# Kernel optimization log

Measured on AMD Instinct MI355X. Metric: run time of the kernel, lower is better.

The kernel has to match this reference:

```python
import jax, jax.numpy as jnp
import numpy as np

RATIO = 0.3
BN_EPS = 1e-5
L2_EPS = 1e-8


def setup_inputs() -> dict:
    key = jax.random.key(0)
    ks = jax.random.split(key, 16)
    B, N, D, E = 128, 577, 512, 1024
    H = E // 2  # mlp hidden = 512
    s = lambda k, shp, fan: jax.random.normal(k, shp, dtype=jnp.float32) * (1.0 / np.sqrt(fan))
    return {
        "features": jax.random.normal(ks[0], (B, N, D), dtype=jnp.float32),
        "atten": jax.random.uniform(ks[1], (B, N), dtype=jnp.float32),
        # image_weight_generator: Linear(D,D) -> ReLU -> Linear(D,1)
        "wg_w1": s(ks[2], (D, D), D), "wg_b1": jnp.zeros((D,), jnp.float32),
        "wg_w2": s(ks[3], (D, 1), D), "wg_b2": jnp.zeros((1,), jnp.float32),
        # fc: Linear(D, E)
        "fc_w": s(ks[4], (D, E), D), "fc_b": jnp.zeros((E,), jnp.float32),
        # MLP: Linear(D,H) -> BN(H) -> ReLU -> Linear(H,E)
        "mlp_w0": s(ks[5], (D, H), D), "mlp_b0": jnp.zeros((H,), jnp.float32),
        "bn_g": jnp.ones((H,), jnp.float32), "bn_b": jnp.zeros((H,), jnp.float32),
        "mlp_w1": s(ks[6], (H, E), H), "mlp_b1": jnp.zeros((E,), jnp.float32),
    }


def reference(features, atten, wg_w1, wg_b1, wg_w2, wg_b2, fc_w, fc_b,
              mlp_w0, mlp_b0, bn_g, bn_b, mlp_w1, mlp_b1):
    k = int((atten.shape[1] - 1) * RATIO)  # static: int(576*0.3)=172
    # weight-generator MLP -> per-token scalar weights [B, N]
    h = jax.nn.relu(jnp.einsum('bnd,de->bne', features, wg_w1) + wg_b1)
    w = (jnp.einsum('bnd,do->bno', h, wg_w2) + wg_b2)[..., 0]
    w = w.at[:, 0].set(-jnp.inf)  # mask CLS token
    w = jax.nn.softmax(w, axis=1)
    # top-k token selection (sorted indices), batched gather
    _, idx = jax.lax.top_k(w, k)                      # [B, k]
    idx = jnp.sort(idx, axis=1)
    sel = jnp.take_along_axis(features, idx[:, :, None], axis=1)  # [B, k, D]
    # l2norm over feature dim
    norm = jnp.sqrt(jnp.sum(sel * sel, axis=-1, keepdims=True)) + L2_EPS
    sel = sel / norm
    # fc in half precision (original: fc(selected_tokens.half()))
    feats = (sel.astype(jnp.float16) @ fc_w.astype(jnp.float16)
             + fc_b.astype(jnp.float16))              # [B, k, E] fp16
    # MLP with training-mode BatchNorm over flattened (B*k) dim
    B, K, D = sel.shape
    x = sel.reshape(B * K, D) @ mlp_w0 + mlp_b0       # [B*k, H]
    mean = jnp.mean(x, axis=0)
    var = jnp.mean((x - mean) ** 2, axis=0)
    x = (x - mean) * jax.lax.rsqrt(var + BN_EPS) * bn_g + bn_b
    x = jax.nn.relu(x)
    x = (x @ mlp_w1 + mlp_b1).reshape(B, K, -1)       # [B, k, E]
    return (x + feats.astype(jnp.float32)).astype(jnp.float32)
```

## Files before the change

### kernel.cpp

```cpp
#include <hip/hip_runtime.h>
#include <hip/hip_fp16.h>
#include <math.h>

#define B_    128
#define NTOK  577
#define KSEL  172
#define M_WG  (B_*NTOK)
#define M_SEL (B_*KSEL)
#define DELTA 8e-3f

typedef float f32x4 __attribute__((ext_vector_type(4)));
typedef short s16x8 __attribute__((ext_vector_type(8)));
typedef short s16x4 __attribute__((ext_vector_type(4)));
typedef _Float16 f16x8 __attribute__((ext_vector_type(8)));

__device__ __forceinline__ void gll16(const void* g, void* l) {
    __builtin_amdgcn_global_load_lds(
        (const __attribute__((address_space(1))) unsigned int*)g,
        (__attribute__((address_space(3))) unsigned int*)l, 16, 0, 0);
}

__global__ void zero_kernel(float* __restrict__ w, float* __restrict__ stats) {
    int i = blockIdx.x * 256 + threadIdx.x;
    if (i < M_WG) w[i] = 0.f;
    if (i < 1024) stats[i] = 0.f;
}

__global__ __launch_bounds__(256) void transpose_f16_kernel(
    const float* __restrict__ wgw1, const float* __restrict__ mw0,
    const float* __restrict__ mw1, const float* __restrict__ fcw,
    short* __restrict__ w1t, short* __restrict__ w0t,
    short* __restrict__ mw1t, short* __restrict__ fct)
{
    const int z = blockIdx.z;
    const float* src; short* dst; int N;
    if (z == 0)      { src = wgw1; dst = w1t;  N = 512;  }
    else if (z == 1) { src = mw0;  dst = w0t;  N = 512;  }
    else if (z == 2) { src = mw1;  dst = mw1t; N = 1024; }
    else             { src = fcw;  dst = fct;  N = 1024; }
    const int n0 = blockIdx.x * 64;
    if (n0 >= N) return;
    const int k0 = blockIdx.y * 64;
    __shared__ float t[64][65];
    const int tid = threadIdx.x;
#pragma unroll
    for (int rr = 0; rr < 16; rr++) {
        int kl = rr * 4 + (tid >> 6), nl = tid & 63;
        t[kl][nl] = src[(size_t)(k0 + kl) * N + n0 + nl];
    }
    __syncthreads();
    const int nl = tid >> 2, kc = tid & 3;
    short hs[16];
#pragma unroll
    for (int j = 0; j < 16; j++)
        hs[j] = (short)__half_as_ushort(__float2half(t[kc * 16 + j][nl]));
    size_t o = (size_t)(n0 + nl) * 512 + k0 + kc * 16;
    *(s16x8*)(dst + o)     = *(s16x8*)hs;
    *(s16x8*)(dst + o + 8) = *(s16x8*)(hs + 8);
}

__global__ __launch_bounds__(256) void wg_f16_kernel(
    const float* __restrict__ F, const short* __restrict__ W1t,
    const float* __restrict__ b1, const float* __restrict__ v,
    float* __restrict__ w_out)
{
    __shared__ short A2[2][4096];
    __shared__ short B2[2][8192];
    const int tid = threadIdx.x, lane = tid & 63, wn = tid >> 6;
    const int r = lane & 15, kq = lane >> 4;
    const int rowbase = blockIdx.y * 128, nbase = blockIdx.x * 256;
    float av[2][8];

    {
        int k0 = 0;
#pragma unroll
        for (int p = 0; p < 4; p++) {
            int c = tid + p * 256, col = c & 255, kqs = c >> 8;
            gll16(W1t + (size_t)(nbase + col) * 512 + k0 + kqs * 8, &B2[0][c * 8]);
        }
#pragma unroll
        for (int p = 0; p < 2; p++) {
            int c = tid + p * 256, row = c & 127, kqs = c >> 7;
            const float* s = F + (size_t)(rowbase + row) * 512 + k0 + kqs * 8;
            f32x4 u0 = *(const f32x4*)s, u1 = *(const f32x4*)(s + 4);
#pragma unroll
            for (int j = 0; j < 4; j++) { av[p][j] = u0[j]; av[p][4 + j] = u1[j]; }
            short hs[8];
#pragma unroll
            for (int j = 0; j < 8; j++) hs[j] = (short)__half_as_ushort(__float2half(av[p][j]));
            *(s16x8*)&A2[0][kqs * 1024 + row * 8] = *(s16x8*)hs;
        }
    }
    __syncthreads();

    f32x4 acc[8][4];
#pragma unroll
    for (int i = 0; i < 8; i++)
#pragma unroll
        for (int j = 0; j < 4; j++) acc[i][j] = (f32x4)(0.0f);

    for (int km = 0; km < 16; km++) {
        const int pb = km & 1;
        if (km < 15) {
            int k0 = (km + 1) * 32;
#pragma unroll
            for (int p = 0; p < 4; p++) {
                int c = tid + p * 256, col = c & 255, kqs = c >> 8;
                gll16(W1t + (size_t)(nbase + col) * 512 + k0 + kqs * 8, &B2[pb ^ 1][c * 8]);
            }
#pragma unroll
            for (int p = 0; p < 2; p++) {
                int c = tid + p * 256, row = c & 127, kqs = c >> 7;
                const float* s = F + (size_t)(rowbase + row) * 512 + k0 + kqs * 8;
                f32x4 u0 = *(const f32x4*)s, u1 = *(const f32x4*)(s + 4);
#pragma unroll
                for (int j = 0; j < 4; j++) { av[p][j] = u0[j]; av[p][4 + j] = u1[j]; }
            }
        }
        f16x8 bfrag[4];
#pragma unroll
        for (int nf = 0; nf < 4; nf++)
            bfrag[nf] = *(const f16x8*)&B2[pb][kq * 2048 + (wn * 64 + nf * 16 + r) * 8];
#pragma unroll
        for (int mf = 0; mf < 8; mf++) {
            f16x8 a = *(const f16x8*)&A2[pb][kq * 1024 + (mf * 16 + r) * 8];
#pragma unroll
            for (int nf = 0; nf < 4; nf++)
                acc[mf][nf] = __builtin_amdgcn_mfma_f32_16x16x32_f16(a, bfrag[nf], acc[mf][nf], 0, 0, 0);
        }
        if (km < 15) {
#pragma unroll
            for (int p = 0; p < 2; p++) {
                int c = tid + p * 256, row = c & 127, kqs = c >> 7;
                short hs[8];
#pragma unroll
                for (int j = 0; j < 8; j++) hs[j] = (short)__half_as_ushort(__float2half(av[p][j]));
                *(s16x8*)&A2[pb ^ 1][kqs * 1024 + row * 8] = *(s16x8*)hs;
            }
        }
        __syncthreads();
    }

    float b1v[4], vv[4];
#pragma unroll
    for (int nf = 0; nf < 4; nf++) {
        int col = nbase + wn * 64 + nf * 16 + r;
        b1v[nf] = b1[col]; vv[nf] = v[col];
    }
#pragma unroll
    for (int mf = 0; mf < 8; mf++)
#pragma unroll
        for (int i = 0; i < 4; i++) {
            float s = 0.f;
#pragma unroll
            for (int nf = 0; nf < 4; nf++)
                s += fmaxf(acc[mf][nf][i] + b1v[nf], 0.f) * vv[nf];
            s += __shfl_xor(s, 1); s += __shfl_xor(s, 2);
            s += __shfl_xor(s, 4); s += __shfl_xor(s, 8);
            if (r == 0)
                atomicAdd(&w_out[rowbase + mf * 16 + kq * 4 + i], s);
        }
}

__global__ __launch_bounds__(512) void topk2_kernel(
    const float* __restrict__ w, int* __restrict__ cin, int* __restrict__ unc,
    int* __restrict__ meta)
{
    __shared__ float sval[1024];
    __shared__ int   sidx[1024];
    __shared__ int mcnt, ucnt;
    __shared__ float thr_s;
    const int b = blockIdx.x;
    const int tid = threadIdx.x;
    for (int i = tid; i < 1024; i += 512) {
        if (i < 576) { sval[i] = w[b * NTOK + 1 + i]; sidx[i] = 1 + i; }
        else         { sval[i] = -1e38f;              sidx[i] = 0x7fffffff; }
    }
    __syncthreads();
    for (int ksz = 2; ksz <= 1024; ksz <<= 1) {
        for (int j = ksz >> 1; j > 0; j >>= 1) {
            int i = ((tid & ~(j - 1)) << 1) | (tid & (j - 1));
            int ixj = i | j;
            float va = sval[i], vb = sval[ixj];
            int ia = sidx[i], ib = sidx[ixj];
            bool a_first = (va > vb) || (va == vb && ia < ib);
            bool dirDesc = ((i & ksz) == 0);
            bool doswap = dirDesc ? (!a_first) : a_first;
            if (doswap) { sval[i] = vb; sval[ixj] = va; sidx[i] = ib; sidx[ixj] = ia; }
            __syncthreads();
        }
    }
    if (tid == 0) { thr_s = sval[KSEL - 1]; mcnt = 0; ucnt = 0; }
    __syncthreads();
    const float thr = thr_s;
    for (int i = tid; i < 576; i += 512) {
        float vv = sval[i]; int id = sidx[i];
        if (vv > thr + DELTA) {
            int p = atomicAdd(&mcnt, 1);
            cin[b * KSEL + p] = id;
        } else if (vv >= thr - DELTA) {
            int p = atomicAdd(&ucnt, 1);
            if (p < 256) unc[b * 256 + p] = id;
        }
    }
    __syncthreads();
    if (tid == 0) {
        int m = mcnt;
        int u = (ucnt < 256) ? ucnt : 256;
        meta[b * 4]     = m;
        meta[b * 4 + 1] = KSEL - m;
        meta[b * 4 + 2] = u;
    }
}

__global__ __launch_bounds__(256) void refine_kernel(
    const float* __restrict__ F, const float* __restrict__ W1,
    const float* __restrict__ b1, const float* __restrict__ v,
    const int* __restrict__ unc, const int* __restrict__ meta,
    float* __restrict__ rscore)
{
    const int b = blockIdx.y, tid = threadIdx.x;
    const int u = meta[b * 4 + 2];
    __shared__ float fr[512];
    __shared__ float redbuf[4];
    for (int s = blockIdx.x; s < u; s += 32) {
        int tok = unc[b * 256 + s];
        __syncthreads();
        fr[tid]       = F[((size_t)b * NTOK + tok) * 512 + tid];
        fr[tid + 256] = F[((size_t)b * NTOK + tok) * 512 + tid + 256];
        __syncthreads();
        float a0 = b1[tid], a1 = b1[tid + 256];
#pragma unroll 4
        for (int k = 0; k < 512; k++) {
            float fk = fr[k];
            a0 = fmaf(fk, W1[(size_t)k * 512 + tid], a0);
            a1 = fmaf(fk, W1[(size_t)k * 512 + tid + 256], a1);
        }
        float p = fmaxf(a0, 0.f) * v[tid] + fmaxf(a1, 0.f) * v[tid + 256];
#pragma unroll
        for (int off = 32; off > 0; off >>= 1) p += __shfl_down(p, off);
        if ((tid & 63) == 0) redbuf[tid >> 6] = p;
        __syncthreads();
        if (tid == 0) rscore[b * 256 + s] = redbuf[0] + redbuf[1] + redbuf[2] + redbuf[3];
    }
}

__global__ __launch_bounds__(256) void select_kernel(
    const int* __restrict__ cin, const int* __restrict__ unc,
    const float* __restrict__ rscore, const int* __restrict__ meta,
    int* __restrict__ idx_out)
{
    const int b = blockIdx.x, tid = threadIdx.x;
    const int m = meta[b * 4], u = meta[b * 4 + 2];
    __shared__ float uval[256];
    __shared__ int   uidx[256];
    __shared__ int   fin[256];
    if (tid < u) { uval[tid] = rscore[b * 256 + tid]; uidx[tid] = unc[b * 256 + tid]; }
    else         { uval[tid] = -1e38f;                uidx[tid] = 0x7fffffff; }
    __syncthreads();
    for (int ksz = 2; ksz <= 256; ksz <<= 1) {
        for (int j = ksz >> 1; j > 0; j >>= 1) {
            if (tid < 128) {
                int i = ((tid & ~(j - 1)) << 1) | (tid & (j - 1));
                int ixj = i | j;
                float va = uval[i], vb = uval[ixj];
                int ia = uidx[i], ib = uidx[ixj];
                bool a_first = (va > vb) || (va == vb && ia < ib);
                bool dirDesc = ((i & ksz) == 0);
                if (dirDesc ? !a_first : a_first) {
                    uval[i] = vb; uval[ixj] = va; uidx[i] = ib; uidx[ixj] = ia;
                }
            }
            __syncthreads();
        }
    }
    if (tid < m) fin[tid] = cin[b * KSEL + tid];
    else if (tid < KSEL) fin[tid] = uidx[tid - m];
    else fin[tid] = 0x7fffffff;
    __syncthreads();
    for (int ksz = 2; ksz <= 256; ksz <<= 1) {
        for (int j = ksz >> 1; j > 0; j >>= 1) {
            if (tid < 128) {
                int i = ((tid & ~(j - 1)) << 1) | (tid & (j - 1));
                int ixj = i | j;
                int a = fin[i], bb = fin[ixj];
                bool asc = ((i & ksz) == 0);
                if (asc ? (a > bb) : (a < bb)) { fin[i] = bb; fin[ixj] = a; }
            }
            __syncthreads();
        }
    }
    if (tid < KSEL) idx_out[b * KSEL + tid] = fin[tid];
}

__global__ __launch_bounds__(128) void gather_norm_kernel(
    const float* __restrict__ F, const int* __restrict__ idx,
    short* __restrict__ Sh)
{
    const int g = blockIdx.x;
    const int b = g / KSEL;
    const int tok = idx[g];
    const float4* src = (const float4*)(F + ((size_t)b * NTOK + tok) * 512);
    const int t = threadIdx.x;
    float4 v = src[t];
    float ss = v.x * v.x + v.y * v.y + v.z * v.z + v.w * v.w;
#pragma unroll
    for (int off = 32; off > 0; off >>= 1) ss += __shfl_down(ss, off);
    __shared__ float red[2];
    if ((t & 63) == 0) red[t >> 6] = ss;
    __syncthreads();
    float inv = 1.0f / (sqrtf(red[0] + red[1]) + 1e-8f);
    float xs[4] = {v.x * inv, v.y * inv, v.z * inv, v.w * inv};
    short hs[4];
#pragma unroll
    for (int j = 0; j < 4; j++) hs[j] = (short)__half_as_ushort(__float2half(xs[j]));
    *(s16x4*)(Sh + (size_t)g * 512 + t * 4) = *(s16x4*)hs;
}

__global__ __launch_bounds__(256) void gemm_x1_kernel(
    const short* __restrict__ Sh, const short* __restrict__ W0t,
    const float* __restrict__ b0, short* __restrict__ X1h, float* __restrict__ stats)
{
    __shared__ short A[4096], Bt[8192];
    const int tid = threadIdx.x, lane = tid & 63, wn = tid >> 6;
    const int rowbase = blockIdx.y * 128, nbase = blockIdx.x * 256;
    const int r = lane & 15, kq = lane >> 4;
    f32x4 acc[8][4];
#pragma unroll
    for (int i = 0; i < 8; i++)
#pragma unroll
        for (int j = 0; j < 4; j++) acc[i][j] = (f32x4)(0.0f);
    for (int k0 = 0; k0 < 512; k0 += 32) {
#pragma unroll
        for (int p = 0; p < 2; p++) {
            int c = tid + p * 256, row = c & 127, kqs = c >> 7;
            gll16(Sh + (size_t)(rowbase + row) * 512 + k0 + kqs * 8, A + c * 8);
        }
#pragma unroll
        for (int p = 0; p < 4; p++) {
            int c = tid + p * 256, col = c & 255, kqs = c >> 8;
            gll16(W0t + (size_t)(nbase + col) * 512 + k0 + kqs * 8, Bt + c * 8);
        }
        __syncthreads();
        f16x8 b[4];
#pragma unroll
        for (int nf = 0; nf < 4; nf++)
            b[nf] = *(const f16x8*)(Bt + kq * 2048 + (wn * 64 + nf * 16 + r) * 8);
#pragma unroll
        for (int mf = 0; mf < 8; mf++) {
            f16x8 a = *(const f16x8*)(A + kq * 1024 + (mf * 16 + r) * 8);
#pragma unroll
            for (int nf = 0; nf < 4; nf++)
                acc[mf][nf] = __builtin_amdgcn_mfma_f32_16x16x32_f16(a, b[nf], acc[mf][nf], 0, 0, 0);
        }
        __syncthreads();
    }
#pragma unroll
    for (int nf = 0; nf < 4; nf++) {
        int col = nbase + wn * 64 + nf * 16 + r;
        float b0v = b0[col];
        float cs = 0.f, cq = 0.f;
#pragma unroll
        for (int mf = 0; mf < 8; mf++)
#pragma unroll
            for (int i = 0; i < 4; i++) {
                int row = rowbase + mf * 16 + kq * 4 + i;
                float val = acc[mf][nf][i] + b0v;
                X1h[(size_t)row * 512 + col] = (short)__half_as_ushort(__float2half(val));
                cs += val; cq += val * val;
            }
        cs += __shfl_xor(cs, 16); cs += __shfl_xor(cs, 32);
        cq += __shfl_xor(cq, 16); cq += __shfl_xor(cq, 32);
        if (kq == 0) {
            atomicAdd(&stats[col], cs);
            atomicAdd(&stats[512 + col], cq);
        }
    }
}

__global__ void bn_finalize_kernel(const float* __restrict__ stats,
                                   const float* __restrict__ g,
                                   const float* __restrict__ b,
                                   float* __restrict__ ss)
{
    int c = threadIdx.x;
    float mean = stats[c] * (1.0f / M_SEL);
    float var = stats[512 + c] * (1.0f / M_SEL) - mean * mean;
    float sc = g[c] * rsqrtf(var + 1e-5f);
    ss[c] = sc;
    ss[512 + c] = b[c] - mean * sc;
}

__global__ __launch_bounds__(256) void gemm_out2_kernel(
    const short* __restrict__ Sh, const short* __restrict__ FCt,
    const float* __restrict__ fcb, const short* __restrict__ X1h,
    const short* __restrict__ W1t, const float* __restrict__ ssbuf,
    const float* __restrict__ b1, float* __restrict__ out)
{
    __shared__ short A2[2][4096];
    __shared__ short B2[2][8192];
    __shared__ float sc[512], sh_[512];
    const int tid = threadIdx.x, lane = tid & 63, wn = tid >> 6;
    const int rowbase = blockIdx.y * 128, nbase = blockIdx.x * 256;
    const int r = lane & 15, kq = lane >> 4;
    for (int i = tid; i < 512; i += 256) { sc[i] = ssbuf[i]; sh_[i] = ssbuf[512 + i]; }
    f32x4 acc[8][4];
#pragma unroll
    for (int i = 0; i < 8; i++)
#pragma unroll
        for (int j = 0; j < 4; j++) acc[i][j] = (f32x4)(0.0f);

    {
#pragma unroll
        for (int p = 0; p < 2; p++) {
            int c = tid + p * 256, row = c & 127, kqs = c >> 7;
            gll16(Sh + (size_t)(rowbase + row) * 512 + kqs * 8, &A2[0][c * 8]);
        }
#pragma unroll
        for (int p = 0; p < 4; p++) {
            int c = tid + p * 256, col = c & 255, kqs = c >> 8;
            gll16(FCt + (size_t)(nbase + col) * 512 + kqs * 8, &B2[0][c * 8]);
        }
    }
    __syncthreads();
    for (int km = 0; km < 16; km++) {
        const int pb = km & 1;
        if (km < 15) {
            int k0 = (km + 1) * 32;
#pragma unroll
            for (int p = 0; p < 2; p++) {
                int c = tid + p * 256, row = c & 127, kqs = c >> 7;
                gll16(Sh + (size_t)(rowbase + row) * 512 + k0 + kqs * 8, &A2[pb ^ 1][c * 8]);
            }
#pragma unroll
            for (int p = 0; p < 4; p++) {
                int c = tid + p * 256, col = c & 255, kqs = c >> 8;
                gll16(FCt + (size_t)(nbase + col) * 512 + k0 + kqs * 8, &B2[pb ^ 1][c * 8]);
            }
        }
        f16x8 b[4];
#pragma unroll
        for (int nf = 0; nf < 4; nf++)
            b[nf] = *(const f16x8*)&B2[pb][kq * 2048 + (wn * 64 + nf * 16 + r) * 8];
#pragma unroll
        for (int mf = 0; mf < 8; mf++) {
            f16x8 a = *(const f16x8*)&A2[pb][kq * 1024 + (mf * 16 + r) * 8];
#pragma unroll
            for (int nf = 0; nf < 4; nf++)
                acc[mf][nf] = __builtin_amdgcn_mfma_f32_16x16x32_f16(a, b[nf], acc[mf][nf], 0, 0, 0);
        }
        __syncthreads();
    }
#pragma unroll
    for (int nf = 0; nf < 4; nf++) {
        float fb = __half2float(__float2half(fcb[nbase + wn * 64 + nf * 16 + r]));
#pragma unroll
        for (int mf = 0; mf < 8; mf++)
#pragma unroll
            for (int i = 0; i < 4; i++) {
                float t = __half2float(__float2half(acc[mf][nf][i]));
                acc[mf][nf][i] = __half2float(__float2half(t + fb));
            }
    }

    s16x8 xv[2];
    {
#pragma unroll
        for (int p = 0; p < 2; p++) {
            int c = tid + p * 256, row = c & 127, kqs = c >> 7;
            xv[p] = *(const s16x8*)(X1h + (size_t)(rowbase + row) * 512 + kqs * 8);
        }
#pragma unroll
        for (int p = 0; p < 2; p++) {
            int c = tid + p * 256, row = c & 127, kqs = c >> 7;
            short hs[8];
#pragma unroll
            for (int j = 0; j < 8; j++) {
                float xf = __half2float(__ushort_as_half((unsigned short)xv[p][j]));
                int k = kqs * 8 + j;
                hs[j] = (short)__half_as_ushort(__float2half(fmaxf(fmaf(xf, sc[k], sh_[k]), 0.f)));
            }
            *(s16x8*)&A2[0][kqs * 1024 + row * 8] = *(s16x8*)hs;
        }
#pragma unroll
        for (int p = 0; p < 4; p++) {
            int c = tid + p * 256, col = c & 255, kqs = c >> 8;
            gll16(W1t + (size_t)(nbase + col) * 512 + kqs * 8, &B2[0][c * 8]);
        }
    }
    __syncthreads();
    for (int km = 0; km < 16; km++) {
        const int pb = km & 1;
        if (km < 15) {
            int k0 = (km + 1) * 32;
#pragma unroll
            for (int p = 0; p < 4; p++) {
                int c = tid + p * 256, col = c & 255, kqs = c >> 8;
                gll16(W1t + (size_t)(nbase + col) * 512 + k0 + kqs * 8, &B2[pb ^ 1][c * 8]);
            }
#pragma unroll
            for (int p = 0; p < 2; p++) {
                int c = tid + p * 256, row = c & 127, kqs = c >> 7;
                xv[p] = *(const s16x8*)(X1h + (size_t)(rowbase + row) * 512 + k0 + kqs * 8);
            }
        }
        f16x8 b[4];
#pragma unroll
        for (int nf = 0; nf < 4; nf++)
            b[nf] = *(const f16x8*)&B2[pb][kq * 2048 + (wn * 64 + nf * 16 + r) * 8];
#pragma unroll
        for (int mf = 0; mf < 8; mf++) {
            f16x8 a = *(const f16x8*)&A2[pb][kq * 1024 + (mf * 16 + r) * 8];
#pragma unroll
            for (int nf = 0; nf < 4; nf++)
                acc[mf][nf] = __builtin_amdgcn_mfma_f32_16x16x32_f16(a, b[nf], acc[mf][nf], 0, 0, 0);
        }
        if (km < 15) {
            int k0 = (km + 1) * 32;
#pragma unroll
            for (int p = 0; p < 2; p++) {
                int c = tid + p * 256, row = c & 127, kqs = c >> 7;
                short hs[8];
#pragma unroll
                for (int j = 0; j < 8; j++) {
                    float xf = __half2float(__ushort_as_half((unsigned short)xv[p][j]));
                    int k = k0 + kqs * 8 + j;
                    hs[j] = (short)__half_as_ushort(__float2half(fmaxf(fmaf(xf, sc[k], sh_[k]), 0.f)));
                }
                *(s16x8*)&A2[pb ^ 1][kqs * 1024 + row * 8] = *(s16x8*)hs;
            }
        }
        __syncthreads();
    }
#pragma unroll
    for (int nf = 0; nf < 4; nf++) {
        int col = nbase + wn * 64 + nf * 16 + r;
        float bb = b1[col];
#pragma unroll
        for (int mf = 0; mf < 8; mf++)
#pragma unroll
            for (int i = 0; i < 4; i++) {
                int row = rowbase + mf * 16 + kq * 4 + i;
                out[(size_t)row * 1024 + col] = acc[mf][nf][i] + bb;
            }
    }
}

extern "C" void kernel_launch(void* const* d_in, const int* in_sizes, int n_in,
                              void* d_out, int out_size, void* d_ws, size_t ws_size,
                              hipStream_t stream)
{
    const float* features = (const float*)d_in[0];
    const float* wg_w1 = (const float*)d_in[2];
    const float* wg_b1 = (const float*)d_in[3];
    const float* wg_w2 = (const float*)d_in[4];
    const float* fc_w  = (const float*)d_in[6];
    const float* fc_b  = (const float*)d_in[7];
    const float* mlp_w0 = (const float*)d_in[8];
    const float* mlp_b0 = (const float*)d_in[9];
    const float* bn_g  = (const float*)d_in[10];
    const float* bn_b  = (const float*)d_in[11];
    const float* mlp_w1 = (const float*)d_in[12];
    const float* mlp_b1 = (const float*)d_in[13];
    float* out = (float*)d_out;

    char* ws = (char*)d_ws;
    float* w_scores  = (float*)(ws + 0);
    float* stats     = (float*)(ws + 295424);
    float* scaleshift= (float*)(ws + 299520);
    int*   meta      = (int*)  (ws + 303616);
    int*   idx_sel   = (int*)  (ws + 305664);
    int*   cin_list  = (int*)  (ws + 393728);
    int*   unc_list  = (int*)  (ws + 481792);
    float* rscore    = (float*)(ws + 612864);
    short* w1t       = (short*)(ws + 743936);
    short* w0t       = (short*)(ws + 1268224);
    short* mw1t      = (short*)(ws + 1792512);
    short* fct       = (short*)(ws + 2841088);
    short* sel_h     = (short*)(ws + 3889664);
    short* x1h       = (short*)(ws + 26434048);

    zero_kernel<<<289, 256, 0, stream>>>(w_scores, stats);
    transpose_f16_kernel<<<dim3(16, 8, 4), 256, 0, stream>>>(
        wg_w1, mlp_w0, mlp_w1, fc_w, w1t, w0t, mw1t, fct);
    wg_f16_kernel<<<dim3(2, 577), 256, 0, stream>>>(
        features, w1t, wg_b1, wg_w2, w_scores);
    topk2_kernel<<<B_, 512, 0, stream>>>(w_scores, cin_list, unc_list, meta);
    refine_kernel<<<dim3(32, B_), 256, 0, stream>>>(
        features, wg_w1, wg_b1, wg_w2, unc_list, meta, rscore);
    select_kernel<<<B_, 256, 0, stream>>>(cin_list, unc_list, rscore, meta, idx_sel);
    gather_norm_kernel<<<M_SEL, 128, 0, stream>>>(features, idx_sel, sel_h);
    gemm_x1_kernel<<<dim3(2, 172), 256, 0, stream>>>(
        sel_h, w0t, mlp_b0, x1h, stats);
    bn_finalize_kernel<<<1, 512, 0, stream>>>(stats, bn_g, bn_b, scaleshift);
    gemm_out2_kernel<<<dim3(4, 172), 256, 0, stream>>>(
        sel_h, fct, fc_b, x1h, mw1t, scaleshift, mlp_b1, out);
}
```

Measured before the change: 761.1 us.

## Pre-convert features to fp16 and concatenate fc/MLP GEMMs along K

```diff
diff --git a/kernel.cpp b/kernel.cpp
--- a/kernel.cpp
+++ b/kernel.cpp
@@ -20,24 +20,37 @@
         (__attribute__((address_space(3))) unsigned int*)l, 16, 0, 0);
 }
 
-__global__ void zero_kernel(float* __restrict__ w, float* __restrict__ stats) {
-    int i = blockIdx.x * 256 + threadIdx.x;
-    if (i < M_WG) w[i] = 0.f;
-    if (i < 1024) stats[i] = 0.f;
+__global__ __launch_bounds__(256) void prep_kernel(
+    const float* __restrict__ F, short* __restrict__ Ff16,
+    float* __restrict__ wsc, float* __restrict__ stats)
+{
+    const int gid = blockIdx.x * 256 + threadIdx.x;
+    const int stride = gridDim.x * 256;
+    const int n4 = M_WG * 512 / 4;
+    for (int i = gid; i < n4; i += stride) {
+        float4 v = *(const float4*)(F + (size_t)i * 4);
+        short hs[4];
+        hs[0] = (short)__half_as_ushort(__float2half(v.x));
+        hs[1] = (short)__half_as_ushort(__float2half(v.y));
+        hs[2] = (short)__half_as_ushort(__float2half(v.z));
+        hs[3] = (short)__half_as_ushort(__float2half(v.w));
+        *(s16x4*)(Ff16 + (size_t)i * 4) = *(s16x4*)hs;
+    }
+    if (gid < M_WG) wsc[gid] = 0.f;
+    if (gid < 1024) stats[gid] = 0.f;
 }
 
 __global__ __launch_bounds__(256) void transpose_f16_kernel(
     const float* __restrict__ wgw1, const float* __restrict__ mw0,
     const float* __restrict__ mw1, const float* __restrict__ fcw,
-    short* __restrict__ w1t, short* __restrict__ w0t,
-    short* __restrict__ mw1t, short* __restrict__ fct)
+    short* __restrict__ w1t, short* __restrict__ w0t, short* __restrict__ BW)
 {
     const int z = blockIdx.z;
-    const float* src; short* dst; int N;
-    if (z == 0)      { src = wgw1; dst = w1t;  N = 512;  }
-    else if (z == 1) { src = mw0;  dst = w0t;  N = 512;  }
-    else if (z == 2) { src = mw1;  dst = mw1t; N = 1024; }
-    else             { src = fcw;  dst = fct;  N = 1024; }
+    const float* src; short* dst; int N, dstride, koff;
+    if (z == 0)      { src = wgw1; dst = w1t; N = 512;  dstride = 512;  koff = 0; }
+    else if (z == 1) { src = mw0;  dst = w0t; N = 512;  dstride = 512;  koff = 0; }
+    else if (z == 2) { src = mw1;  dst = BW;  N = 1024; dstride = 1024; koff = 512; }
+    else             { src = fcw;  dst = BW;  N = 1024; dstride = 1024; koff = 0; }
     const int n0 = blockIdx.x * 64;
     if (n0 >= N) return;
     const int k0 = blockIdx.y * 64;
@@ -54,93 +67,60 @@
 #pragma unroll
     for (int j = 0; j < 16; j++)
         hs[j] = (short)__half_as_ushort(__float2half(t[kc * 16 + j][nl]));
-    size_t o = (size_t)(n0 + nl) * 512 + k0 + kc * 16;
+    size_t o = (size_t)(n0 + nl) * dstride + koff + k0 + kc * 16;
     *(s16x8*)(dst + o)     = *(s16x8*)hs;
     *(s16x8*)(dst + o + 8) = *(s16x8*)(hs + 8);
 }
 
+__device__ __forceinline__ void gemm_core(
+    const short* __restrict__ Ag, int strideA, int rowbase,
+    const short* __restrict__ Bg, int strideB, int nbase, int Ktot,
+    int tid, short* Als, short* Bls, f32x4 acc[8][4])
+{
+    const int lane = tid & 63, wn = tid >> 6;
+    const int r = lane & 15, kq = lane >> 4;
+    for (int k0 = 0; k0 < Ktot; k0 += 32) {
+#pragma unroll
+        for (int p = 0; p < 2; p++) {
+            int c = tid + p * 256, row = c & 127, kqs = c >> 7;
+            gll16(Ag + (size_t)(rowbase + row) * strideA + k0 + kqs * 8, Als + c * 8);
+        }
+#pragma unroll
+        for (int p = 0; p < 4; p++) {
+            int c = tid + p * 256, col = c & 255, kqs = c >> 8;
+            gll16(Bg + (size_t)(nbase + col) * strideB + k0 + kqs * 8, Bls + c * 8);
+        }
+        __syncthreads();
+        f16x8 bf[4];
+#pragma unroll
+        for (int nf = 0; nf < 4; nf++)
+            bf[nf] = *(const f16x8*)(Bls + kq * 2048 + (wn * 64 + nf * 16 + r) * 8);
+#pragma unroll
+        for (int mf = 0; mf < 8; mf++) {
+            f16x8 a = *(const f16x8*)(Als + kq * 1024 + (mf * 16 + r) * 8);
+#pragma unroll
+            for (int nf = 0; nf < 4; nf++)
+                acc[mf][nf] = __builtin_amdgcn_mfma_f32_16x16x32_f16(a, bf[nf], acc[mf][nf], 0, 0, 0);
+        }
+        __syncthreads();
+    }
+}
+
 __global__ __launch_bounds__(256) void wg_f16_kernel(
-    const float* __restrict__ F, const short* __restrict__ W1t,
+    const short* __restrict__ Ff16, const short* __restrict__ W1t,
     const float* __restrict__ b1, const float* __restrict__ v,
     float* __restrict__ w_out)
 {
-    __shared__ short A2[2][4096];
-    __shared__ short B2[2][8192];
+    __shared__ short Als[4096], Bls[8192];
     const int tid = threadIdx.x, lane = tid & 63, wn = tid >> 6;
     const int r = lane & 15, kq = lane >> 4;
     const int rowbase = blockIdx.y * 128, nbase = blockIdx.x * 256;
-    float av[2][8];
-
-    {
-        int k0 = 0;
-#pragma unroll
-        for (int p = 0; p < 4; p++) {
-            int c = tid + p * 256, col = c & 255, kqs = c >> 8;
-            gll16(W1t + (size_t)(nbase + col) * 512 + k0 + kqs * 8, &B2[0][c * 8]);
-        }
-#pragma unroll
-        for (int p = 0; p < 2; p++) {
-            int c = tid + p * 256, row = c & 127, kqs = c >> 7;
-            const float* s = F + (size_t)(rowbase + row) * 512 + k0 + kqs * 8;
-            f32x4 u0 = *(const f32x4*)s, u1 = *(const f32x4*)(s + 4);
-#pragma unroll
-            for (int j = 0; j < 4; j++) { av[p][j] = u0[j]; av[p][4 + j] = u1[j]; }
-            short hs[8];
-#pragma unroll
-            for (int j = 0; j < 8; j++) hs[j] = (short)__half_as_ushort(__float2half(av[p][j]));
-            *(s16x8*)&A2[0][kqs * 1024 + row * 8] = *(s16x8*)hs;
-        }
-    }
-    __syncthreads();
-
     f32x4 acc[8][4];
 #pragma unroll
     for (int i = 0; i < 8; i++)
 #pragma unroll
         for (int j = 0; j < 4; j++) acc[i][j] = (f32x4)(0.0f);
-
-    for (int km = 0; km < 16; km++) {
-        const int pb = km & 1;
-        if (km < 15) {
-            int k0 = (km + 1) * 32;
-#pragma unroll
-            for (int p = 0; p < 4; p++) {
-                int c = tid + p * 256, col = c & 255, kqs = c >> 8;
-                gll16(W1t + (size_t)(nbase + col) * 512 + k0 + kqs * 8, &B2[pb ^ 1][c * 8]);
-            }
-#pragma unroll
-            for (int p = 0; p < 2; p++) {
-                int c = tid + p * 256, row = c & 127, kqs = c >> 7;
-                const float* s = F + (size_t)(rowbase + row) * 512 + k0 + kqs * 8;
-                f32x4 u0 = *(const f32x4*)s, u1 = *(const f32x4*)(s + 4);
-#pragma unroll
-                for (int j = 0; j < 4; j++) { av[p][j] = u0[j]; av[p][4 + j] = u1[j]; }
-            }
-        }
-        f16x8 bfrag[4];
-#pragma unroll
-        for (int nf = 0; nf < 4; nf++)
-            bfrag[nf] = *(const f16x8*)&B2[pb][kq * 2048 + (wn * 64 + nf * 16 + r) * 8];
-#pragma unroll
-        for (int mf = 0; mf < 8; mf++) {
-            f16x8 a = *(const f16x8*)&A2[pb][kq * 1024 + (mf * 16 + r) * 8];
-#pragma unroll
-            for (int nf = 0; nf < 4; nf++)
-                acc[mf][nf] = __builtin_amdgcn_mfma_f32_16x16x32_f16(a, bfrag[nf], acc[mf][nf], 0, 0, 0);
-        }
-        if (km < 15) {
-#pragma unroll
-            for (int p = 0; p < 2; p++) {
-                int c = tid + p * 256, row = c & 127, kqs = c >> 7;
-                short hs[8];
-#pragma unroll
-                for (int j = 0; j < 8; j++) hs[j] = (short)__half_as_ushort(__float2half(av[p][j]));
-                *(s16x8*)&A2[pb ^ 1][kqs * 1024 + row * 8] = *(s16x8*)hs;
-            }
-        }
-        __syncthreads();
-    }
-
+    gemm_core(Ff16, 512, rowbase, W1t, 512, nbase, 512, tid, Als, Bls, acc);
     float b1v[4], vv[4];
 #pragma unroll
     for (int nf = 0; nf < 4; nf++) {
@@ -295,7 +275,7 @@
 
 __global__ __launch_bounds__(128) void gather_norm_kernel(
     const float* __restrict__ F, const int* __restrict__ idx,
-    short* __restrict__ Sh)
+    short* __restrict__ AY)
 {
     const int g = blockIdx.x;
     const int b = g / KSEL;
@@ -314,47 +294,23 @@
     short hs[4];
 #pragma unroll
     for (int j = 0; j < 4; j++) hs[j] = (short)__half_as_ushort(__float2half(xs[j]));
-    *(s16x4*)(Sh + (size_t)g * 512 + t * 4) = *(s16x4*)hs;
+    *(s16x4*)(AY + (size_t)g * 1024 + t * 4) = *(s16x4*)hs;
 }
 
 __global__ __launch_bounds__(256) void gemm_x1_kernel(
-    const short* __restrict__ Sh, const short* __restrict__ W0t,
-    const float* __restrict__ b0, short* __restrict__ X1h, float* __restrict__ stats)
-{
-    __shared__ short A[4096], Bt[8192];
+    short* __restrict__ AY, const short* __restrict__ W0t,
+    const float* __restrict__ b0, float* __restrict__ stats)
+{
+    __shared__ short Als[4096], Bls[8192];
     const int tid = threadIdx.x, lane = tid & 63, wn = tid >> 6;
+    const int r = lane & 15, kq = lane >> 4;
     const int rowbase = blockIdx.y * 128, nbase = blockIdx.x * 256;
-    const int r = lane & 15, kq = lane >> 4;
     f32x4 acc[8][4];
 #pragma unroll
     for (int i = 0; i < 8; i++)
 #pragma unroll
         for (int j = 0; j < 4; j++) acc[i][j] = (f32x4)(0.0f);
-    for (int k0 = 0; k0 < 512; k0 += 32) {
-#pragma unroll
-        for (int p = 0; p < 2; p++) {
-            int c = tid + p * 256, row = c & 127, kqs = c >> 7;
-            gll16(Sh + (size_t)(rowbase + row) * 512 + k0 + kqs * 8, A + c * 8);
-        }
-#pragma unroll
-        for (int p = 0; p < 4; p++) {
-            int c = tid + p * 256, col = c & 255, kqs = c >> 8;
-            gll16(W0t + (size_t)(nbase + col) * 512 + k0 + kqs * 8, Bt + c * 8);
-        }
-        __syncthreads();
-        f16x8 b[4];
-#pragma unroll
-        for (int nf = 0; nf < 4; nf++)
-            b[nf] = *(const f16x8*)(Bt + kq * 2048 + (wn * 64 + nf * 16 + r) * 8);
-#pragma unroll
-        for (int mf = 0; mf < 8; mf++) {
-            f16x8 a = *(const f16x8*)(A + kq * 1024 + (mf * 16 + r) * 8);
-#pragma unroll
-            for (int nf = 0; nf < 4; nf++)
-                acc[mf][nf] = __builtin_amdgcn_mfma_f32_16x16x32_f16(a, b[nf], acc[mf][nf], 0, 0, 0);
-        }
-        __syncthreads();
-    }
+    gemm_core(AY, 1024, rowbase, W0t, 512, nbase, 512, tid, Als, Bls, acc);
 #pragma unroll
     for (int nf = 0; nf < 4; nf++) {
         int col = nbase + wn * 64 + nf * 16 + r;
@@ -366,7 +322,7 @@
             for (int i = 0; i < 4; i++) {
                 int row = rowbase + mf * 16 + kq * 4 + i;
                 float val = acc[mf][nf][i] + b0v;
-                X1h[(size_t)row * 512 + col] = (short)__half_as_ushort(__float2half(val));
+                AY[(size_t)row * 1024 + 512 + col] = (short)__half_as_ushort(__float2half(val));
                 cs += val; cq += val * val;
             }
         cs += __shfl_xor(cs, 16); cs += __shfl_xor(cs, 32);
@@ -391,151 +347,46 @@
     ss[512 + c] = b[c] - mean * sc;
 }
 
+__global__ __launch_bounds__(256) void bn_apply_kernel(
+    short* __restrict__ AY, const float* __restrict__ ss)
+{
+    const int stride = gridDim.x * 256;
+    const int ng = M_SEL * 512 / 8;
+    for (int g = blockIdx.x * 256 + threadIdx.x; g < ng; g += stride) {
+        int row = g >> 6, cg = g & 63;
+        size_t o = (size_t)row * 1024 + 512 + cg * 8;
+        s16x8 xv = *(const s16x8*)(AY + o);
+        short hs[8];
+#pragma unroll
+        for (int j = 0; j < 8; j++) {
+            int k = cg * 8 + j;
+            float xf = __half2float(__ushort_as_half((unsigned short)xv[j]));
+            float y = fmaxf(fmaf(xf, ss[k], ss[512 + k]), 0.f);
+            hs[j] = (short)__half_as_ushort(__float2half(y));
+        }
+        *(s16x8*)(AY + o) = *(s16x8*)hs;
+    }
+}
+
 __global__ __launch_bounds__(256) void gemm_out2_kernel(
-    const short* __restrict__ Sh, const short* __restrict__ FCt,
-    const float* __restrict__ fcb, const short* __restrict__ X1h,
-    const short* __restrict__ W1t, const float* __restrict__ ssbuf,
-    const float* __restrict__ b1, float* __restrict__ out)
-{
-    __shared__ short A2[2][4096];
-    __shared__ short B2[2][8192];
-    __shared__ float sc[512], sh_[512];
+    const short* __restrict__ AY, const short* __restrict__ BW,
+    const float* __restrict__ fcb, const float* __restrict__ b1m,
+    float* __restrict__ out)
+{
+    __shared__ short Als[4096], Bls[8192];
     const int tid = threadIdx.x, lane = tid & 63, wn = tid >> 6;
+    const int r = lane & 15, kq = lane >> 4;
     const int rowbase = blockIdx.y * 128, nbase = blockIdx.x * 256;
-    const int r = lane & 15, kq = lane >> 4;
-    for (int i = tid; i < 512; i += 256) { sc[i] = ssbuf[i]; sh_[i] = ssbuf[512 + i]; }
     f32x4 acc[8][4];
 #pragma unroll
     for (int i = 0; i < 8; i++)
 #pragma unroll
         for (int j = 0; j < 4; j++) acc[i][j] = (f32x4)(0.0f);
-
-    {
-#pragma unroll
-        for (int p = 0; p < 2; p++) {
-            int c = tid + p * 256, row = c & 127, kqs = c >> 7;
-            gll16(Sh + (size_t)(rowbase + row) * 512 + kqs * 8, &A2[0][c * 8]);
-        }
-#pragma unroll
-        for (int p = 0; p < 4; p++) {
-            int c = tid + p * 256, col = c & 255, kqs = c >> 8;
-            gll16(FCt + (size_t)(nbase + col) * 512 + kqs * 8, &B2[0][c * 8]);
-        }
-    }
-    __syncthreads();
-    for (int km = 0; km < 16; km++) {
-        const int pb = km & 1;
-        if (km < 15) {
-            int k0 = (km + 1) * 32;
-#pragma unroll
-            for (int p = 0; p < 2; p++) {
-                int c = tid + p * 256, row = c & 127, kqs = c >> 7;
-                gll16(Sh + (size_t)(rowbase + row) * 512 + k0 + kqs * 8, &A2[pb ^ 1][c * 8]);
-            }
-#pragma unroll
-            for (int p = 0; p < 4; p++) {
-                int c = tid + p * 256, col = c & 255, kqs = c >> 8;
-                gll16(FCt + (size_t)(nbase + col) * 512 + k0 + kqs * 8, &B2[pb ^ 1][c * 8]);
-            }
-        }
-        f16x8 b[4];
-#pragma unroll
-        for (int nf = 0; nf < 4; nf++)
-            b[nf] = *(const f16x8*)&B2[pb][kq * 2048 + (wn * 64 + nf * 16 + r) * 8];
-#pragma unroll
-        for (int mf = 0; mf < 8; mf++) {
-            f16x8 a = *(const f16x8*)&A2[pb][kq * 1024 + (mf * 16 + r) * 8];
-#pragma unroll
-            for (int nf = 0; nf < 4; nf++)
-                acc[mf][nf] = __builtin_amdgcn_mfma_f32_16x16x32_f16(a, b[nf], acc[mf][nf], 0, 0, 0);
-        }
-        __syncthreads();
-    }
-#pragma unroll
-    for (int nf = 0; nf < 4; nf++) {
-        float fb = __half2float(__float2half(fcb[nbase + wn * 64 + nf * 16 + r]));
-#pragma unroll
-        for (int mf = 0; mf < 8; mf++)
-#pragma unroll
-            for (int i = 0; i < 4; i++) {
-                float t = __half2float(__float2half(acc[mf][nf][i]));
-                acc[mf][nf][i] = __half2float(__float2half(t + fb));
-            }
-    }
-
-    s16x8 xv[2];
-    {
-#pragma unroll
-        for (int p = 0; p < 2; p++) {
-            int c = tid + p * 256, row = c & 127, kqs = c >> 7;
-            xv[p] = *(const s16x8*)(X1h + (size_t)(rowbase + row) * 512 + kqs * 8);
-        }
-#pragma unroll
-        for (int p = 0; p < 2; p++) {
-            int c = tid + p * 256, row = c & 127, kqs = c >> 7;
-            short hs[8];
-#pragma unroll
-            for (int j = 0; j < 8; j++) {
-                float xf = __half2float(__ushort_as_half((unsigned short)xv[p][j]));
-                int k = kqs * 8 + j;
-                hs[j] = (short)__half_as_ushort(__float2half(fmaxf(fmaf(xf, sc[k], sh_[k]), 0.f)));
-            }
-            *(s16x8*)&A2[0][kqs * 1024 + row * 8] = *(s16x8*)hs;
-        }
-#pragma unroll
-        for (int p = 0; p < 4; p++) {
-            int c = tid + p * 256, col = c & 255, kqs = c >> 8;
-            gll16(W1t + (size_t)(nbase + col) * 512 + kqs * 8, &B2[0][c * 8]);
-        }
-    }
-    __syncthreads();
-    for (int km = 0; km < 16; km++) {
-        const int pb = km & 1;
-        if (km < 15) {
-            int k0 = (km + 1) * 32;
-#pragma unroll
-            for (int p = 0; p < 4; p++) {
-                int c = tid + p * 256, col = c & 255, kqs = c >> 8;
-                gll16(W1t + (size_t)(nbase + col) * 512 + k0 + kqs * 8, &B2[pb ^ 1][c * 8]);
-            }
-#pragma unroll
-            for (int p = 0; p < 2; p++) {
-                int c = tid + p * 256, row = c & 127, kqs = c >> 7;
-                xv[p] = *(const s16x8*)(X1h + (size_t)(rowbase + row) * 512 + k0 + kqs * 8);
-            }
-        }
-        f16x8 b[4];
-#pragma unroll
-        for (int nf = 0; nf < 4; nf++)
-            b[nf] = *(const f16x8*)&B2[pb][kq * 2048 + (wn * 64 + nf * 16 + r) * 8];
-#pragma unroll
-        for (int mf = 0; mf < 8; mf++) {
-            f16x8 a = *(const f16x8*)&A2[pb][kq * 1024 + (mf * 16 + r) * 8];
-#pragma unroll
-            for (int nf = 0; nf < 4; nf++)
-                acc[mf][nf] = __builtin_amdgcn_mfma_f32_16x16x32_f16(a, b[nf], acc[mf][nf], 0, 0, 0);
-        }
-        if (km < 15) {
-            int k0 = (km + 1) * 32;
-#pragma unroll
-            for (int p = 0; p < 2; p++) {
-                int c = tid + p * 256, row = c & 127, kqs = c >> 7;
-                short hs[8];
-#pragma unroll
-                for (int j = 0; j < 8; j++) {
-                    float xf = __half2float(__ushort_as_half((unsigned short)xv[p][j]));
-                    int k = k0 + kqs * 8 + j;
-                    hs[j] = (short)__half_as_ushort(__float2half(fmaxf(fmaf(xf, sc[k], sh_[k]), 0.f)));
-                }
-                *(s16x8*)&A2[pb ^ 1][kqs * 1024 + row * 8] = *(s16x8*)hs;
-            }
-        }
-        __syncthreads();
-    }
+    gemm_core(AY, 1024, rowbase, BW, 1024, nbase, 1024, tid, Als, Bls, acc);
 #pragma unroll
     for (int nf = 0; nf < 4; nf++) {
         int col = nbase + wn * 64 + nf * 16 + r;
-        float bb = b1[col];
+        float bb = __half2float(__float2half(fcb[col])) + b1m[col];
 #pragma unroll
         for (int mf = 0; mf < 8; mf++)
 #pragma unroll
@@ -575,24 +426,23 @@
     float* rscore    = (float*)(ws + 612864);
     short* w1t       = (short*)(ws + 743936);
     short* w0t       = (short*)(ws + 1268224);
-    short* mw1t      = (short*)(ws + 1792512);
-    short* fct       = (short*)(ws + 2841088);
-    short* sel_h     = (short*)(ws + 3889664);
-    short* x1h       = (short*)(ws + 26434048);
-
-    zero_kernel<<<289, 256, 0, stream>>>(w_scores, stats);
+    short* BW        = (short*)(ws + 1792512);
+    short* Ff16      = (short*)(ws + 3889664);
+    short* AY        = (short*)(ws + 3889664);
+
+    prep_kernel<<<2048, 256, 0, stream>>>(features, Ff16, w_scores, stats);
     transpose_f16_kernel<<<dim3(16, 8, 4), 256, 0, stream>>>(
-        wg_w1, mlp_w0, mlp_w1, fc_w, w1t, w0t, mw1t, fct);
+        wg_w1, mlp_w0, mlp_w1, fc_w, w1t, w0t, BW);
     wg_f16_kernel<<<dim3(2, 577), 256, 0, stream>>>(
-        features, w1t, wg_b1, wg_w2, w_scores);
+        Ff16, w1t, wg_b1, wg_w2, w_scores);
     topk2_kernel<<<B_, 512, 0, stream>>>(w_scores, cin_list, unc_list, meta);
     refine_kernel<<<dim3(32, B_), 256, 0, stream>>>(
         features, wg_w1, wg_b1, wg_w2, unc_list, meta, rscore);
     select_kernel<<<B_, 256, 0, stream>>>(cin_list, unc_list, rscore, meta, idx_sel);
-    gather_norm_kernel<<<M_SEL, 128, 0, stream>>>(features, idx_sel, sel_h);
-    gemm_x1_kernel<<<dim3(2, 172), 256, 0, stream>>>(
-        sel_h, w0t, mlp_b0, x1h, stats);
+    gather_norm_kernel<<<M_SEL, 128, 0, stream>>>(features, idx_sel, AY);
+    gemm_x1_kernel<<<dim3(2, 172), 256, 0, stream>>>(AY, w0t, mlp_b0, stats);
     bn_finalize_kernel<<<1, 512, 0, stream>>>(stats, bn_g, bn_b, scaleshift);
+    bn_apply_kernel<<<1024, 256, 0, stream>>>(AY, scaleshift);
     gemm_out2_kernel<<<dim3(4, 172), 256, 0, stream>>>(
-        sel_h, fct, fc_b, x1h, mw1t, scaleshift, mlp_b1, out);
-}
+        AY, BW, fc_b, mlp_b1, out);
+}
```

Measured after the change: 789.2 us. +3.7%, slower.
